# Performance work log

Measured on AMD Instinct MI355X. Metric: run time of the kernel, lower is better.

## Reference

```python
import jax, jax.numpy as jnp
import numpy as np

EPS = 1e-5
N_HEADS, N_KV, HEAD_DIM = 32, 2, 128


def rms_norm(x, w):
    var = jnp.mean(jnp.square(x.astype(jnp.float32)), axis=-1, keepdims=True)
    return (w * (x * jax.lax.rsqrt(var + EPS))).astype(x.dtype)


def apply_rope(x, cache):
    # x: [sq, b, np, hn], cache: [sq, rot/2, 2]
    sq, b, nh, hn = x.shape
    rot = cache.shape[-2] * 2
    xr, xp = x[..., :rot], x[..., rot:]
    xr = xr.reshape(sq, b, nh, rot // 2, 2)
    c = cache[:sq].reshape(sq, 1, 1, rot // 2, 2)
    out = jnp.stack([
        xr[..., 0] * c[..., 0] - xr[..., 1] * c[..., 1],
        xr[..., 1] * c[..., 0] + xr[..., 0] * c[..., 1],
    ], axis=-1).reshape(sq, b, nh, rot)
    return jnp.concatenate([out, xp], axis=-1)


def expand_kv(x, sq, b):
    # [sq, b, n_kv, hd] -> [sq, b, n_heads, hd] by repeating each kv head
    reps = N_HEADS // N_KV
    return jnp.broadcast_to(x[:, :, :, None, :], (sq, b, N_KV, reps, HEAD_DIM)).reshape(sq, b, N_HEADS, HEAD_DIM)


def causal_attention(q, k, v):
    # q,k,v: [b, h, s, d]
    s = q.shape[2]
    scale = 1.0 / np.sqrt(q.shape[-1]).astype(np.float32)
    scores = jnp.einsum('bhqd,bhkd->bhqk', q, k) * scale
    mask = jnp.tril(jnp.ones((s, s), dtype=bool))
    scores = jnp.where(mask, scores, jnp.float32(-1e30))
    attn = jax.nn.softmax(scores, axis=-1)
    return jnp.einsum('bhqk,bhkd->bhqd', attn, v)


def setup_inputs() -> dict:
    key = jax.random.key(0)
    ks = jax.random.split(key, 8)
    sq, b, h = 2048, 1, 4096
    inp = {
        'hidden_states': jax.random.normal(ks[0], (sq, b, h), jnp.float32),
        'rope_cache': jax.random.normal(ks[1], (sq, 32, 2), jnp.float32),
        'w_ln1': jnp.ones((h,), jnp.float32),
        'w_qkv': jax.random.normal(ks[2], (4608, h), jnp.float32) * 0.02,
        'b_qkv': jax.random.normal(ks[3], (4608,), jnp.float32) * 0.02,
        'w_dense': jax.random.normal(ks[4], (h, h), jnp.float32) * 0.02,
        'w_ln2': jnp.ones((h,), jnp.float32),
        'w_h4h': jax.random.normal(ks[5], (27392, h), jnp.float32) * 0.02,
        'w_4hh': jax.random.normal(ks[6], (h, 13696), jnp.float32) * 0.02,
    }
    return inp


def reference(hidden_states, rope_cache, w_ln1, w_qkv, b_qkv, w_dense, w_ln2, w_h4h, w_4hh):
    sq, b, h = hidden_states.shape
    ln1 = rms_norm(hidden_states, w_ln1)
    mixed = ln1 @ w_qkv.T + b_qkv  # [sq, b, 4608]
    q = mixed[..., : N_HEADS * HEAD_DIM].reshape(sq, b, N_HEADS, HEAD_DIM)
    k = mixed[..., N_HEADS * HEAD_DIM: (N_HEADS + N_KV) * HEAD_DIM].reshape(sq, b, N_KV, HEAD_DIM)
    v = mixed[..., (N_HEADS + N_KV) * HEAD_DIM:].reshape(sq, b, N_KV, HEAD_DIM)
    q = apply_rope(q, rope_cache)
    k = apply_rope(k, rope_cache)
    k = expand_kv(k, sq, b)
    v = expand_kv(v, sq, b)
    # [sq, b, h, d] -> [b, h, sq, d]
    q, k, v = (t.transpose(1, 2, 0, 3) for t in (q, k, v))
    ctx = causal_attention(q, k, v)  # [b, h, sq, d]
    ctx = ctx.transpose(2, 0, 1, 3).reshape(sq, b, N_HEADS * HEAD_DIM)
    attn_out = ctx @ w_dense.T
    ln_in = hidden_states + attn_out
    ln2 = rms_norm(ln_in, w_ln2)
    inter = ln2 @ w_h4h.T  # [sq, b, 27392]
    a, g = jnp.split(inter, 2, axis=-1)
    mlp = (jax.nn.silu(a) * g) @ w_4hh.T
    return ln_in + mlp
```

## Files before the change

### kernel.cpp

```cpp
#include <hip/hip_runtime.h>

typedef __bf16 bf16x8 __attribute__((ext_vector_type(8)));
typedef float f32x4 __attribute__((ext_vector_type(4)));
typedef unsigned short us8 __attribute__((ext_vector_type(8)));
typedef unsigned short us4 __attribute__((ext_vector_type(4)));

__device__ __forceinline__ unsigned short f2bf(float f) {
  unsigned u = __builtin_bit_cast(unsigned, f);
  u += 0x7FFFu + ((u >> 16) & 1u);
  return (unsigned short)(u >> 16);
}
__device__ __forceinline__ float bf2f(unsigned short h) {
  return __builtin_bit_cast(float, (unsigned)h << 16);
}
__device__ __forceinline__ void glds16(const void* g, void* l) {
  __builtin_amdgcn_global_load_lds(
      (__attribute__((address_space(1))) void*)g,
      (__attribute__((address_space(3))) void*)l, 16, 0, 0);
}

__global__ __launch_bounds__(256) void cvt_bf16(const float* __restrict__ in,
                                                unsigned short* __restrict__ out,
                                                long n8) {
  const long stride = (long)gridDim.x * 256;
  for (long c = (long)blockIdx.x * 256 + threadIdx.x; c < n8; c += stride) {
    const float4 a = ((const float4*)in)[c * 2];
    const float4 b = ((const float4*)in)[c * 2 + 1];
    us8 u;
    u[0] = f2bf(a.x); u[1] = f2bf(a.y); u[2] = f2bf(a.z); u[3] = f2bf(a.w);
    u[4] = f2bf(b.x); u[5] = f2bf(b.y); u[6] = f2bf(b.z); u[7] = f2bf(b.w);
    ((us8*)out)[c] = u;
  }
}

__global__ __launch_bounds__(256) void rmsnorm_k(const float* __restrict__ x,
                                                 const float* __restrict__ wgt,
                                                 unsigned short* __restrict__ out) {
  const int r = blockIdx.x, t = threadIdx.x;
  const float* xr = x + (long)r * 4096;
  float4 vv[4];
  float ss = 0.f;
#pragma unroll
  for (int i = 0; i < 4; ++i) {
    float4 v = ((const float4*)xr)[t + i * 256];
    vv[i] = v;
    ss += v.x * v.x + v.y * v.y + v.z * v.z + v.w * v.w;
  }
#pragma unroll
  for (int off = 1; off < 64; off <<= 1) ss += __shfl_xor(ss, off);
  __shared__ float ps[4];
  if ((t & 63) == 0) ps[t >> 6] = ss;
  __syncthreads();
  ss = ps[0] + ps[1] + ps[2] + ps[3];
  const float rinv = rsqrtf(ss * (1.f / 4096.f) + 1e-5f);
#pragma unroll
  for (int i = 0; i < 4; ++i) {
    const int c4 = t + i * 256;
    const float4 v = vv[i];
    const float4 g = ((const float4*)wgt)[c4];
    us4 u;
    u[0] = f2bf(v.x * rinv * g.x);
    u[1] = f2bf(v.y * rinv * g.y);
    u[2] = f2bf(v.z * rinv * g.z);
    u[3] = f2bf(v.w * rinv * g.w);
    *(us4*)(out + (long)r * 4096 + c4 * 4) = u;
  }
}

template <int MODE>
__global__ __launch_bounds__(256)
void gemm_nt(const unsigned short* __restrict__ A,
             const unsigned short* __restrict__ B,
             void* __restrict__ outp, const void* __restrict__ extra,
             int M, int N, int K) {
  __shared__ unsigned short lsA[128 * 64];
  __shared__ unsigned short lsB[128 * 64];
  const int t = threadIdx.x;
  const int l = t & 63, w = t >> 6;
  const int fr = l & 15, fq = l >> 4;
  const int wr = w >> 1, wc = w & 1;
  const int bm0 = blockIdx.x * 128, bn0 = blockIdx.y * 128;
  const int stgrow = w * 8 + (l >> 3);
  const int stgch = (l & 7) ^ (l >> 3);

  f32x4 acc[4][4] = {};

  for (int k0 = 0; k0 < K; k0 += 64) {
#pragma unroll
    for (int i = 0; i < 4; ++i) {
      glds16(A + (long)(bm0 + i * 32 + stgrow) * K + k0 + stgch * 8,
             (char*)lsA + i * 4096 + w * 1024);
      glds16(B + (long)(bn0 + i * 32 + stgrow) * K + k0 + stgch * 8,
             (char*)lsB + i * 4096 + w * 1024);
    }
    __syncthreads();
#pragma unroll
    for (int kk = 0; kk < 2; ++kk) {
      bf16x8 av[4], bv[4];
#pragma unroll
      for (int mi = 0; mi < 4; ++mi) {
        const int row = wr * 64 + mi * 16 + fr;
        const int ch = (kk * 4 + fq) ^ (fr & 7);
        av[mi] = *reinterpret_cast<const bf16x8*>((const char*)lsA + row * 128 + ch * 16);
      }
#pragma unroll
      for (int ni = 0; ni < 4; ++ni) {
        const int row = wc * 64 + ni * 16 + fr;
        const int ch = (kk * 4 + fq) ^ (fr & 7);
        bv[ni] = *reinterpret_cast<const bf16x8*>((const char*)lsB + row * 128 + ch * 16);
      }
#pragma unroll
      for (int mi = 0; mi < 4; ++mi)
#pragma unroll
        for (int ni = 0; ni < 4; ++ni)
          acc[mi][ni] = __builtin_amdgcn_mfma_f32_16x16x32_bf16(av[mi], bv[ni], acc[mi][ni], 0, 0, 0);
    }
    __syncthreads();
  }

#pragma unroll
  for (int mi = 0; mi < 4; ++mi) {
#pragma unroll
    for (int ni = 0; ni < 4; ++ni) {
      const int col = bn0 + wc * 64 + ni * 16 + fr;
      const int row0 = bm0 + wr * 64 + mi * 16 + fq * 4;
      if constexpr (MODE == 0) {
        float* O = (float*)outp;
        const float b = ((const float*)extra)[col];
#pragma unroll
        for (int j = 0; j < 4; ++j)
          O[(long)(row0 + j) * N + col] = acc[mi][ni][j] + b;
      } else if constexpr (MODE == 1) {
        float* O = (float*)outp;
#pragma unroll
        for (int j = 0; j < 4; ++j)
          O[(long)(row0 + j) * N + col] = acc[mi][ni][j] + ((const float*)extra)[(long)(row0 + j) * N + col];
      } else if constexpr (MODE == 2) {
        unsigned short* O = (unsigned short*)outp;
#pragma unroll
        for (int j = 0; j < 4; ++j)
          O[(long)(row0 + j) * N + col] = f2bf(acc[mi][ni][j]);
      } else if constexpr (MODE == 3) {
        unsigned short* O = (unsigned short*)outp;
        const float b = ((const float*)extra)[col];
#pragma unroll
        for (int j = 0; j < 4; ++j)
          O[(long)(row0 + j) * N + col] = f2bf(acc[mi][ni][j] + b);
      } else {
        unsigned short* O = (unsigned short*)outp;
        const unsigned short* Abuf = (const unsigned short*)extra;
#pragma unroll
        for (int j = 0; j < 4; ++j) {
          const long idx = (long)(row0 + j) * N + col;
          const float a = bf2f(Abuf[idx]);
          O[idx] = f2bf(acc[mi][ni][j] * a / (1.f + __expf(-a)));
        }
      }
    }
  }
}

__global__ __launch_bounds__(256)
void rope_split(const unsigned short* __restrict__ mixed, const float* __restrict__ cache,
                unsigned short* __restrict__ qr, unsigned short* __restrict__ kr,
                unsigned short* __restrict__ vr) {
  const int s = blockIdx.x, t = threadIdx.x;
  const unsigned short* row = mixed + (long)s * 4608;
  const float* c = cache + (long)s * 64;
  const float SCALE = 0.08838834764831845f;
  for (int p = t; p < 1024; p += 256) {
    const int hq = p >> 5, pr = p & 31;
    const float x0 = bf2f(row[hq * 128 + 2 * pr]), x1 = bf2f(row[hq * 128 + 2 * pr + 1]);
    const float c0 = c[2 * pr], c1 = c[2 * pr + 1];
    unsigned short* qp = qr + ((long)hq * 2048 + s) * 128;
    qp[2 * pr] = f2bf((x0 * c0 - x1 * c1) * SCALE);
    qp[2 * pr + 1] = f2bf((x1 * c0 + x0 * c1) * SCALE);
  }
  for (int i = t; i < 2048; i += 256) {
    const int hq = i >> 6, d = 64 + (i & 63);
    qr[((long)hq * 2048 + s) * 128 + d] = f2bf(bf2f(row[hq * 128 + d]) * SCALE);
  }
  for (int p = t; p < 64; p += 256) {
    const int kh = p >> 5, pr = p & 31;
    const float x0 = bf2f(row[4096 + kh * 128 + 2 * pr]);
    const float x1 = bf2f(row[4096 + kh * 128 + 2 * pr + 1]);
    const float c0 = c[2 * pr], c1 = c[2 * pr + 1];
    unsigned short* kp = kr + ((long)kh * 2048 + s) * 128;
    kp[2 * pr] = f2bf(x0 * c0 - x1 * c1);
    kp[2 * pr + 1] = f2bf(x1 * c0 + x0 * c1);
  }
  for (int i = t; i < 128; i += 256) {
    const int kh = i >> 6, d = 64 + (i & 63);
    kr[((long)kh * 2048 + s) * 128 + d] = row[4096 + kh * 128 + d];
  }
  for (int i = t; i < 256; i += 256) {
    const int kh = i >> 7, d = i & 127;
    vr[((long)kh * 128 + d) * 2048 + s] = row[4352 + kh * 128 + d];
  }
}

__global__ __launch_bounds__(256)
void attn_fwd(const unsigned short* __restrict__ Q,
              const unsigned short* __restrict__ Kv,
              const unsigned short* __restrict__ Vt_g,
              unsigned short* __restrict__ ctx) {
  __shared__ unsigned short Kl[64 * 128];
  __shared__ unsigned short Vt[128 * 64];
  __shared__ unsigned short Pl[4][16 * 68];
  const int t = threadIdx.x, l = t & 63, w = t >> 6;
  const int fr = l & 15, fq = l >> 4;
  const int h = blockIdx.x >> 5, qb = 31 - (blockIdx.x & 31);
  const int kvh = h >> 4;
  const int q0 = qb * 64;

  bf16x8 qa[4];
  {
    const unsigned short* qp = Q + ((long)h * 2048 + q0 + w * 16 + fr) * 128;
#pragma unroll
    for (int cc = 0; cc < 4; ++cc)
      qa[cc] = *reinterpret_cast<const bf16x8*>(qp + cc * 32 + fq * 8);
  }
  float m[4], lsum[4];
  f32x4 o[8] = {};
#pragma unroll
  for (int j = 0; j < 4; ++j) { m[j] = -1e30f; lsum[j] = 0.f; }

  for (int tile = 0; tile <= qb; ++tile) {
    const int kv0 = tile * 64;
#pragma unroll
    for (int i = 0; i < 4; ++i) {
      const int kv = i * 16 + w * 4 + fq;
      glds16(Kv + ((long)kvh * 2048 + kv0 + kv) * 128 + (fr ^ (kv & 7)) * 8,
             (char*)Kl + i * 4096 + w * 1024);
    }
#pragma unroll
    for (int i = 0; i < 4; ++i) {
      const int d = i * 32 + w * 8 + (l >> 3);
      glds16(Vt_g + ((long)kvh * 128 + d) * 2048 + kv0 + (((l & 7) ^ (l >> 3)) * 8),
             (char*)Vt + i * 4096 + w * 1024);
    }
    __syncthreads();

    f32x4 sc4[4] = {};
#pragma unroll
    for (int ni = 0; ni < 4; ++ni) {
      const int kvr = ni * 16 + fr;
      const int swz = kvr & 7;
#pragma unroll
      for (int cc = 0; cc < 4; ++cc) {
        bf16x8 kb = *reinterpret_cast<const bf16x8*>((const char*)Kl + kvr * 256 + ((cc * 4 + fq) ^ swz) * 16);
        sc4[ni] = __builtin_amdgcn_mfma_f32_16x16x32_bf16(qa[cc], kb, sc4[ni], 0, 0, 0);
      }
    }
    if (tile == qb) {
#pragma unroll
      for (int ni = 0; ni < 4; ++ni)
#pragma unroll
        for (int j = 0; j < 4; ++j)
          if (ni * 16 + fr > w * 16 + fq * 4 + j) sc4[ni][j] = -1e30f;
    }
#pragma unroll
    for (int j = 0; j < 4; ++j) {
      float v = fmaxf(fmaxf(sc4[0][j], sc4[1][j]), fmaxf(sc4[2][j], sc4[3][j]));
#pragma unroll
      for (int off = 1; off < 16; off <<= 1) v = fmaxf(v, __shfl_xor(v, off));
      const float mn = fmaxf(m[j], v);
      const float sc = __expf(m[j] - mn);
      m[j] = mn;
      float r = 0.f;
#pragma unroll
      for (int ni = 0; ni < 4; ++ni) {
        const float p = __expf(sc4[ni][j] - mn);
        sc4[ni][j] = p;
        r += p;
      }
#pragma unroll
      for (int off = 1; off < 16; off <<= 1) r += __shfl_xor(r, off);
      lsum[j] = lsum[j] * sc + r;
#pragma unroll
      for (int d = 0; d < 8; ++d) o[d][j] *= sc;
    }
#pragma unroll
    for (int ni = 0; ni < 4; ++ni)
#pragma unroll
      for (int j = 0; j < 4; ++j)
        Pl[w][(fq * 4 + j) * 68 + ni * 16 + fr] = f2bf(sc4[ni][j]);
#pragma unroll
    for (int kk = 0; kk < 2; ++kk) {
      bf16x8 pa = *reinterpret_cast<const bf16x8*>((const char*)&Pl[w][0] + fr * 136 + kk * 64 + fq * 16);
#pragma unroll
      for (int dj = 0; dj < 8; ++dj) {
        const int d = dj * 16 + fr;
        bf16x8 vb = *reinterpret_cast<const bf16x8*>((const char*)Vt + d * 128 + (((kk * 4 + fq) ^ (d & 7)) << 4));
        o[dj] = __builtin_amdgcn_mfma_f32_16x16x32_bf16(pa, vb, o[dj], 0, 0, 0);
      }
    }
    __syncthreads();
  }

#pragma unroll
  for (int j = 0; j < 4; ++j) {
    const float inv = 1.f / lsum[j];
    const long srow = q0 + w * 16 + fq * 4 + j;
#pragma unroll
    for (int dj = 0; dj < 8; ++dj)
      ctx[srow * 4096 + h * 128 + dj * 16 + fr] = f2bf(o[dj][j] * inv);
  }
}

extern "C" void kernel_launch(void* const* d_in, const int* in_sizes, int n_in,
                              void* d_out, int out_size, void* d_ws, size_t ws_size,
                              hipStream_t stream) {
  (void)in_sizes; (void)n_in; (void)out_size; (void)ws_size;
  const float* hidden = (const float*)d_in[0];
  const float* rope_c = (const float*)d_in[1];
  const float* w_ln1 = (const float*)d_in[2];
  const float* w_qkv = (const float*)d_in[3];
  const float* b_qkv = (const float*)d_in[4];
  const float* w_dense = (const float*)d_in[5];
  const float* w_ln2 = (const float*)d_in[6];
  const float* w_h4h = (const float*)d_in[7];
  const float* w_4hh = (const float*)d_in[8];
  float* out = (float*)d_out;

  char* ws = (char*)d_ws;
  const size_t MB = 1024 * 1024;
  unsigned short* wbuf = (unsigned short*)ws;
  float* lnin = (float*)(ws + 112197632);
  char* lnslot = ws + 112197632 + 33554432;
  char* slotA = lnslot + 16777216;
  char* slotB = slotA + 56098816;
  unsigned short* ln1 = (unsigned short*)lnslot;
  unsigned short* ln2 = ln1;
  unsigned short* mixed = (unsigned short*)slotA;
  unsigned short* interA = (unsigned short*)slotA;
  unsigned short* act = interA;
  unsigned short* qr = (unsigned short*)slotB;
  unsigned short* kr = (unsigned short*)(slotB + 16 * MB);
  unsigned short* vr = (unsigned short*)(slotB + 17 * MB);
  unsigned short* ctx = (unsigned short*)(slotB + 18 * MB);

  const dim3 blk(256);
  cvt_bf16<<<2048, blk, 0, stream>>>(w_qkv, wbuf, (long)4608 * 4096 / 8);
  rmsnorm_k<<<2048, blk, 0, stream>>>(hidden, w_ln1, ln1);
  gemm_nt<3><<<dim3(16, 36), blk, 0, stream>>>(ln1, wbuf, mixed, b_qkv, 2048, 4608, 4096);
  rope_split<<<2048, blk, 0, stream>>>(mixed, rope_c, qr, kr, vr);
  attn_fwd<<<1024, blk, 0, stream>>>(qr, kr, vr, ctx);
  cvt_bf16<<<2048, blk, 0, stream>>>(w_dense, wbuf, (long)4096 * 4096 / 8);
  gemm_nt<1><<<dim3(16, 32), blk, 0, stream>>>(ctx, wbuf, lnin, hidden, 2048, 4096, 4096);
  rmsnorm_k<<<2048, blk, 0, stream>>>(lnin, w_ln2, ln2);
  cvt_bf16<<<4096, blk, 0, stream>>>(w_h4h, wbuf, (long)13696 * 4096 / 8);
  gemm_nt<2><<<dim3(16, 107), blk, 0, stream>>>(ln2, wbuf, interA, nullptr, 2048, 13696, 4096);
  cvt_bf16<<<4096, blk, 0, stream>>>(w_h4h + (long)13696 * 4096, wbuf, (long)13696 * 4096 / 8);
  gemm_nt<4><<<dim3(16, 107), blk, 0, stream>>>(ln2, wbuf, act, interA, 2048, 13696, 4096);
  cvt_bf16<<<4096, blk, 0, stream>>>(w_4hh, wbuf, (long)4096 * 13696 / 8);
  gemm_nt<1><<<dim3(16, 32), blk, 0, stream>>>(act, wbuf, out, lnin, 2048, 4096, 13696);
}
```

Before: 2.200 ms.

## Add double-buffered 256x128 GEMM kernel for MLP projections

Adds a new gemm_big kernel with 512 threads, a 256x128 block tile and double-buffered LDS staging through async global-to-LDS loads, so the next K tile is prefetched while MFMAs run on the current one. It also raises wave priority around the MFMA block. The two MLP up-projections and the down-projection now use it with half as many row blocks. The original gemm_nt modes are trimmed to the bias-bf16 and residual-f32 variants still in use. The larger LDS footprint (96KB per block) limits occupancy, and the 8x107 grid gives fewer blocks to fill the CUs.

```diff
diff --git a/kernel.cpp b/kernel.cpp
--- a/kernel.cpp
+++ b/kernel.cpp
@@ -124,13 +124,95 @@
     for (int ni = 0; ni < 4; ++ni) {
       const int col = bn0 + wc * 64 + ni * 16 + fr;
       const int row0 = bm0 + wr * 64 + mi * 16 + fq * 4;
-      if constexpr (MODE == 0) {
+      if constexpr (MODE == 1) {
         float* O = (float*)outp;
+#pragma unroll
+        for (int j = 0; j < 4; ++j)
+          O[(long)(row0 + j) * N + col] = acc[mi][ni][j] + ((const float*)extra)[(long)(row0 + j) * N + col];
+      } else {
+        unsigned short* O = (unsigned short*)outp;
         const float b = ((const float*)extra)[col];
 #pragma unroll
         for (int j = 0; j < 4; ++j)
-          O[(long)(row0 + j) * N + col] = acc[mi][ni][j] + b;
-      } else if constexpr (MODE == 1) {
+          O[(long)(row0 + j) * N + col] = f2bf(acc[mi][ni][j] + b);
+      }
+    }
+  }
+}
+
+template <int MODE>
+__global__ __launch_bounds__(512, 2)
+void gemm_big(const unsigned short* __restrict__ A,
+              const unsigned short* __restrict__ B,
+              void* __restrict__ outp, const void* __restrict__ extra,
+              int M, int N, int K) {
+  __shared__ unsigned short lsA[2][256 * 64];
+  __shared__ unsigned short lsB[2][128 * 64];
+  const int t = threadIdx.x;
+  const int l = t & 63, wid = t >> 6;
+  const int fr = l & 15, fq = l >> 4;
+  const int wr = wid >> 1, wc = wid & 1;
+  const int bm0 = blockIdx.x * 256, bn0 = blockIdx.y * 128;
+  const int srow = t >> 3;
+  const int sch = (t & 7) ^ (srow & 7);
+  const int NT = K >> 6;
+
+  f32x4 acc[4][4] = {};
+
+  auto stage = [&](int b, int tile) {
+    const int k0 = tile << 6;
+#pragma unroll
+    for (int i = 0; i < 4; ++i)
+      glds16(A + (long)(bm0 + i * 64 + srow) * K + k0 + sch * 8,
+             (char*)lsA[b] + i * 8192 + wid * 1024 + (t & 63) * 16);
+#pragma unroll
+    for (int i = 0; i < 2; ++i)
+      glds16(B + (long)(bn0 + i * 64 + srow) * K + k0 + sch * 8,
+             (char*)lsB[b] + i * 8192 + wid * 1024 + (t & 63) * 16);
+  };
+
+  stage(0, 0);
+  for (int tt = 0; tt < NT; ++tt) {
+    const int cur = tt & 1;
+    stage(cur ^ 1, (tt + 1 == NT) ? 0 : tt + 1);
+    asm volatile("s_waitcnt vmcnt(6)" ::: "memory");
+    __builtin_amdgcn_s_barrier();
+    __builtin_amdgcn_sched_barrier(0);
+#pragma unroll
+    for (int kk = 0; kk < 2; ++kk) {
+      bf16x8 av[4], bv[4];
+#pragma unroll
+      for (int mi = 0; mi < 4; ++mi) {
+        const int row = wr * 64 + mi * 16 + fr;
+        const int ch = (kk * 4 + fq) ^ (fr & 7);
+        av[mi] = *reinterpret_cast<const bf16x8*>((const char*)lsA[cur] + row * 128 + ch * 16);
+      }
+#pragma unroll
+      for (int ni = 0; ni < 4; ++ni) {
+        const int row = wc * 64 + ni * 16 + fr;
+        const int ch = (kk * 4 + fq) ^ (fr & 7);
+        bv[ni] = *reinterpret_cast<const bf16x8*>((const char*)lsB[cur] + row * 128 + ch * 16);
+      }
+      __builtin_amdgcn_s_setprio(1);
+#pragma unroll
+      for (int mi = 0; mi < 4; ++mi)
+#pragma unroll
+        for (int ni = 0; ni < 4; ++ni)
+          acc[mi][ni] = __builtin_amdgcn_mfma_f32_16x16x32_bf16(av[mi], bv[ni], acc[mi][ni], 0, 0, 0);
+      __builtin_amdgcn_s_setprio(0);
+    }
+    __builtin_amdgcn_sched_barrier(0);
+    __builtin_amdgcn_s_barrier();
+  }
+  asm volatile("s_waitcnt vmcnt(0)" ::: "memory");
+
+#pragma unroll
+  for (int mi = 0; mi < 4; ++mi) {
+#pragma unroll
+    for (int ni = 0; ni < 4; ++ni) {
+      const int col = bn0 + wc * 64 + ni * 16 + fr;
+      const int row0 = bm0 + wr * 64 + mi * 16 + fq * 4;
+      if constexpr (MODE == 1) {
         float* O = (float*)outp;
 #pragma unroll
         for (int j = 0; j < 4; ++j)
@@ -140,12 +222,6 @@
 #pragma unroll
         for (int j = 0; j < 4; ++j)
           O[(long)(row0 + j) * N + col] = f2bf(acc[mi][ni][j]);
-      } else if constexpr (MODE == 3) {
-        unsigned short* O = (unsigned short*)outp;
-        const float b = ((const float*)extra)[col];
-#pragma unroll
-        for (int j = 0; j < 4; ++j)
-          O[(long)(row0 + j) * N + col] = f2bf(acc[mi][ni][j] + b);
       } else {
         unsigned short* O = (unsigned short*)outp;
         const unsigned short* Abuf = (const unsigned short*)extra;
@@ -340,7 +416,7 @@
   unsigned short* vr = (unsigned short*)(slotB + 17 * MB);
   unsigned short* ctx = (unsigned short*)(slotB + 18 * MB);
 
-  const dim3 blk(256);
+  const dim3 blk(256), blk2(512);
   cvt_bf16<<<2048, blk, 0, stream>>>(w_qkv, wbuf, (long)4608 * 4096 / 8);
   rmsnorm_k<<<2048, blk, 0, stream>>>(hidden, w_ln1, ln1);
   gemm_nt<3><<<dim3(16, 36), blk, 0, stream>>>(ln1, wbuf, mixed, b_qkv, 2048, 4608, 4096);
@@ -350,9 +426,9 @@
   gemm_nt<1><<<dim3(16, 32), blk, 0, stream>>>(ctx, wbuf, lnin, hidden, 2048, 4096, 4096);
   rmsnorm_k<<<2048, blk, 0, stream>>>(lnin, w_ln2, ln2);
   cvt_bf16<<<4096, blk, 0, stream>>>(w_h4h, wbuf, (long)13696 * 4096 / 8);
-  gemm_nt<2><<<dim3(16, 107), blk, 0, stream>>>(ln2, wbuf, interA, nullptr, 2048, 13696, 4096);
+  gemm_big<2><<<dim3(8, 107), blk2, 0, stream>>>(ln2, wbuf, interA, nullptr, 2048, 13696, 4096);
   cvt_bf16<<<4096, blk, 0, stream>>>(w_h4h + (long)13696 * 4096, wbuf, (long)13696 * 4096 / 8);
-  gemm_nt<4><<<dim3(16, 107), blk, 0, stream>>>(ln2, wbuf, act, interA, 2048, 13696, 4096);
+  gemm_big<4><<<dim3(8, 107), blk2, 0, stream>>>(ln2, wbuf, act, interA, 2048, 13696, 4096);
   cvt_bf16<<<4096, blk, 0, stream>>>(w_4hh, wbuf, (long)4096 * 13696 / 8);
-  gemm_nt<1><<<dim3(16, 32), blk, 0, stream>>>(act, wbuf, out, lnin, 2048, 4096, 13696);
-}
+  gemm_big<1><<<dim3(8, 32), blk2, 0, stream>>>(act, wbuf, out, lnin, 2048, 4096, 13696);
+}
```

Measured after the change: 2.358 ms. 7.2% more time.
